# Kernel tuning notes

Hardware: AMD Instinct MI355X
Metric: run time of the kernel (lower is better)

## Reference

```python
import jax, jax.numpy as jnp
import numpy as np

HEADS = 4
DIM_HEAD = 64
MAP_SIZE = 16
SCALE = DIM_HEAD ** (-0.5)


def _split_heads(x):
    # torch rearrange 'b (dim_head heads) h w -> b heads (h w) dim_head'
    B, C, H, W = x.shape
    x = x.reshape(B, DIM_HEAD, HEADS, H * W)
    return jnp.transpose(x, (0, 2, 3, 1))  # [B, heads, N, dim_head]


def _merge_heads(x, H, W):
    # torch rearrange 'b heads (h w) dim_head -> b (dim_head heads) h w'
    B, h, N, d = x.shape
    return jnp.transpose(x, (0, 3, 1, 2)).reshape(B, d * h, H, W)


def setup_inputs() -> dict:
    key = jax.random.key(0)
    ks = jax.random.split(key, 6)
    feat = jax.random.normal(ks[0], (4, 256, 96, 96), jnp.float32)
    semantic_map = jax.random.normal(ks[1], (4, 256, 16, 16), jnp.float32)
    # 1x1 conv weights, shape [out_ch, in_ch]; scaled like fan-in init
    W_feat_qv = 0.05 * jax.random.normal(ks[2], (512, 256), jnp.float32)
    W_map_qv = 0.05 * jax.random.normal(ks[3], (512, 256), jnp.float32)
    W_feat_out = 0.05 * jax.random.normal(ks[4], (256, 256), jnp.float32)
    W_map_out = 0.05 * jax.random.normal(ks[5], (256, 256), jnp.float32)
    return {
        "feat": feat,
        "semantic_map": semantic_map,
        "W_feat_qv": W_feat_qv,
        "W_map_qv": W_map_qv,
        "W_feat_out": W_feat_out,
        "W_map_out": W_map_out,
    }


def reference(feat, semantic_map, W_feat_qv, W_map_qv, W_feat_out, W_map_out):
    B, C, H, W = feat.shape
    # 1x1 convs == per-pixel channel matmuls
    fqv = jnp.einsum("oc,bchw->bohw", W_feat_qv, feat)
    feat_q, feat_v = jnp.split(fqv, 2, axis=1)
    mqv = jnp.einsum("oc,bchw->bohw", W_map_qv, semantic_map)
    map_q, map_v = jnp.split(mqv, 2, axis=1)

    feat_q, feat_v = _split_heads(feat_q), _split_heads(feat_v)  # [B,h,N,d]
    map_q, map_v = _split_heads(map_q), _split_heads(map_v)      # [B,h,M,d]

    attn = jnp.einsum("bhid,bhjd->bhij", feat_q, map_q) * SCALE  # [B,h,N,M]
    feat_map_attn = jax.nn.softmax(attn, axis=-1)  # normalize over map tokens j
    map_feat_attn = jax.nn.softmax(attn, axis=-2)  # normalize over feat tokens i

    feat_o = jnp.einsum("bhij,bhjd->bhid", feat_map_attn, map_v)   # [B,h,N,d]
    map_o = jnp.einsum("bhji,bhjd->bhid", map_feat_attn, feat_v)   # [B,h,M,d]

    feat_o = _merge_heads(feat_o, H, W)
    map_o = _merge_heads(map_o, MAP_SIZE, MAP_SIZE)

    feat_out = jnp.einsum("oc,bchw->bohw", W_feat_out, feat_o)
    map_out = jnp.einsum("oc,bchw->bohw", W_map_out, map_o)
    return feat_out, map_out
```

## Files before the change

### kernel.cpp

```cpp
#include <hip/hip_runtime.h>
#include <stdint.h>

#define DI static __device__ __forceinline__

constexpr int NTOK = 9216;
constexpr float ATT_SCALE = 0.125f;

typedef short bf16x8 __attribute__((ext_vector_type(8)));
typedef float f32x4  __attribute__((ext_vector_type(4)));

DI f32x4 mfma16(bf16x8 a, bf16x8 b, f32x4 c) {
  return __builtin_amdgcn_mfma_f32_16x16x32_bf16(a, b, c, 0, 0, 0);
}

DI float b2f(uint16_t u) { union { uint32_t i; float f; } v; v.i = ((uint32_t)u) << 16; return v.f; }
DI uint16_t f2b(float f) {
  union { float f; uint32_t i; } v; v.f = f;
  uint32_t r = (v.i + 0x7fffu + ((v.i >> 16) & 1u)) >> 16;
  return (uint16_t)r;
}

template<int DT> DI float ld1(const void* p, size_t off) {
  if constexpr (DT) return b2f(((const uint16_t*)p)[off]);
  else              return ((const float*)p)[off];
}
template<int DT> DI void st1(void* p, size_t off, float v) {
  if constexpr (DT) ((uint16_t*)p)[off] = f2b(v);
  else              ((float*)p)[off] = v;
}

DI int block_flag256(const uint32_t* __restrict__ w) {
  const float b = b2f((uint16_t)(w[threadIdx.x & 255] & 0xffffu));
  const float ab = fabsf(b);
  return (__syncthreads_count((ab > 1e-4f && ab < 0.5f) ? 1 : 0) >= 128) ? 1 : 0;
}

template<int DT>
DI void prep_w_dev(int r, const void* __restrict__ Wfqv, const void* __restrict__ Wfo,
                   uint16_t* __restrict__ WqvP, uint16_t* __restrict__ WfoP)
{
  const int c = threadIdx.x;
  if (r < 512) {
    const int sel = r >> 8, within = r & 255;
    const int h = within >> 6, d = within & 63;
    const int src = sel * 256 + d * 4 + h;
    WqvP[(size_t)r * 256 + c] = f2b(ld1<DT>(Wfqv, (size_t)src * 256 + c));
  } else {
    const int ro = r - 512;
    WfoP[(size_t)ro * 256 + c] =
        f2b(ld1<DT>(Wfo, (size_t)ro * 256 + (c & 63) * 4 + (c >> 6)));
  }
}

template<int DT>
DI void map_qv_dev(int o, int bb, const void* __restrict__ Wqv,
                   const void* __restrict__ smap,
                   uint16_t* __restrict__ MQ, uint16_t* __restrict__ MVT)
{
  const int m = threadIdx.x;
  float acc = 0.f;
  #pragma unroll 8
  for (int c = 0; c < 256; ++c)
    acc += ld1<DT>(Wqv, (size_t)o * 256 + c) *
           ld1<DT>(smap, (size_t)bb * 65536 + (size_t)c * 256 + m);
  const int oc = o & 255;
  const int h = oc & 3, d = oc >> 2;
  if (o < 256) MQ[(((size_t)bb * 4 + h) * 256 + m) * 64 + d] = f2b(acc);
  else         MVT[(((size_t)bb * 4 + h) * 64 + d) * 256 + m] = f2b(acc);
}

__global__ __launch_bounds__(256) void prep_map_k(
    const void* Wfqv, const void* Wfo, const void* Wmqv, const void* smap,
    uint16_t* WqvP, uint16_t* WfoP, uint16_t* MQ, uint16_t* MVT)
{
  const int fl = block_flag256((const uint32_t*)Wfqv);
  const int bid = blockIdx.x;
  if (bid < 768) {
    if (fl) prep_w_dev<1>(bid, Wfqv, Wfo, WqvP, WfoP);
    else    prep_w_dev<0>(bid, Wfqv, Wfo, WqvP, WfoP);
  } else {
    const int idx = bid - 768;
    if (fl) map_qv_dev<1>(idx & 511, idx >> 9, Wmqv, smap, MQ, MVT);
    else    map_qv_dev<0>(idx & 511, idx >> 9, Wmqv, smap, MQ, MVT);
  }
}

constexpr int P0 = 280;

template<int DT>
DI void gemm0_body(uint16_t* Xs, const uint16_t* __restrict__ WqvP,
                   const void* __restrict__ X,
                   uint16_t* __restrict__ FQ, uint16_t* __restrict__ FVt)
{
  const int tid = threadIdx.x;
  const int w = tid >> 6, lane = tid & 63;
  const int l = lane & 15, quad = lane >> 4;
  const int n0 = blockIdx.x * 32;
  const int bb = blockIdx.y;
  const size_t bh = (size_t)bb * 4 + w;

  {
    const int nb = (tid & 15) * 2;
    const int kg = tid >> 4;
    #pragma unroll
    for (int pass = 0; pass < 2; ++pass) {
      const int k0 = pass * 128 + kg * 8;
      union { uint16_t h[8]; uint4 u; } pk0, pk1;
      #pragma unroll
      for (int j = 0; j < 8; ++j) {
        const size_t g = ((size_t)bb * 256 + k0 + j) * NTOK + n0 + nb;
        if constexpr (DT) {
          const uint32_t v = *(const uint32_t*)((const uint16_t*)X + g);
          pk0.h[j] = (uint16_t)(v & 0xffffu);
          pk1.h[j] = (uint16_t)(v >> 16);
        } else {
          const float2 v = *(const float2*)((const float*)X + g);
          pk0.h[j] = f2b(v.x);
          pk1.h[j] = f2b(v.y);
        }
      }
      *(uint4*)(Xs + (size_t)(nb + 0) * P0 + k0) = pk0.u;
      *(uint4*)(Xs + (size_t)(nb + 1) * P0 + k0) = pk1.u;
    }
  }
  __syncthreads();

  f32x4 acc[2][4][2];
  #pragma unroll
  for (int s = 0; s < 2; ++s)
    #pragma unroll
    for (int a = 0; a < 4; ++a)
      #pragma unroll
      for (int b = 0; b < 2; ++b) { acc[s][a][b].x = 0.f; acc[s][a][b].y = 0.f; acc[s][a][b].z = 0.f; acc[s][a][b].w = 0.f; }

  for (int ks = 0; ks < 8; ++ks) {
    bf16x8 bv[2];
    #pragma unroll
    for (int nt = 0; nt < 2; ++nt)
      bv[nt] = *(const bf16x8*)(Xs + (size_t)(nt * 16 + l) * P0 + ks * 32 + quad * 8);
    #pragma unroll
    for (int s = 0; s < 2; ++s) {
      bf16x8 af[4];
      #pragma unroll
      for (int mt = 0; mt < 4; ++mt) {
        const int arow = s * 256 + w * 64 + mt * 16 + l;
        af[mt] = *(const bf16x8*)(WqvP + (size_t)arow * 256 + ks * 32 + quad * 8);
      }
      #pragma unroll
      for (int nt = 0; nt < 2; ++nt)
        #pragma unroll
        for (int mt = 0; mt < 4; ++mt)
          acc[s][mt][nt] = mfma16(af[mt], bv[nt], acc[s][mt][nt]);
    }
  }
  const int itile = blockIdx.x;
  #pragma unroll
  for (int mt = 0; mt < 4; ++mt)
    #pragma unroll
    for (int nt = 0; nt < 2; ++nt) {
      const int n = n0 + nt * 16 + l;
      {
        union { uint16_t h[4]; uint2 u; } pk;
        #pragma unroll
        for (int r = 0; r < 4; ++r) pk.h[r] = f2b(acc[0][mt][nt][r]);
        *(uint2*)(FQ + (bh * NTOK + n) * 64 + mt * 16 + quad * 4) = pk.u;
      }
      {
        const int io = n & 31;
        #pragma unroll
        for (int r = 0; r < 4; ++r)
          FVt[(((size_t)bh * 288 + itile) * 64 + mt * 16 + quad * 4 + r) * 32 + io] =
              f2b(acc[1][mt][nt][r]);
      }
    }
}
__global__ __launch_bounds__(256, 3) void gemm0_mfma(
    const uint16_t* WqvP, const void* X, uint16_t* FQ, uint16_t* FVt,
    const void* Wfqv)
{
  __shared__ __align__(16) uint16_t Xs[32 * P0];
  const int fl = block_flag256((const uint32_t*)Wfqv);
  if (fl) gemm0_body<1>(Xs, WqvP, X, FQ, FVt);
  else    gemm0_body<0>(Xs, WqvP, X, FQ, FVt);
}

constexpr int PJ = 280;
constexpr int PI = 40;
constexpr int PO = 72;
constexpr int NGRP = 48;
constexpr int TPB = 6;

__global__ __launch_bounds__(256, 3) void attn_mfma(
    const uint16_t* __restrict__ FQ, const uint16_t* __restrict__ FVt,
    const uint16_t* __restrict__ MQ, const uint16_t* __restrict__ MVT,
    uint16_t* __restrict__ FO, uint16_t* __restrict__ P,
    uint16_t* __restrict__ CSp)
{
  __shared__ __align__(16) uint16_t Esh[32 * PJ];
  __shared__ __align__(16) uint16_t ETsh[256 * PI];
  __shared__ __align__(16) uint16_t Osh[32 * PO];
  __shared__ float RS[4][32];
  const int tid = threadIdx.x;
  const int w = tid >> 6;
  const int lane = tid & 63;
  const int l = lane & 15, quad = lane >> 4;
  const int blk = blockIdx.x, bh = blockIdx.y;
  const uint16_t* FQh  = FQ  + (size_t)bh * NTOK * 64;
  const uint16_t* FVth = FVt + (size_t)bh * 288 * 64 * 32;
  const uint16_t* MQh  = MQ  + (size_t)bh * 256 * 64;
  const uint16_t* MVTh = MVT + (size_t)bh * 64 * 256;
  uint16_t* FOh = FO + (size_t)bh * NTOK * 64;

  bf16x8 kb[4][2];
  #pragma unroll
  for (int jt = 0; jt < 4; ++jt) {
    const int j = w * 64 + jt * 16 + l;
    kb[jt][0] = *(const bf16x8*)(MQh + (size_t)j * 64 + quad * 8);
    kb[jt][1] = *(const bf16x8*)(MQh + (size_t)j * 64 + 32 + quad * 8);
  }
  bf16x8 avr[8];
  #pragma unroll
  for (int ks = 0; ks < 8; ++ks)
    avr[ks] = *(const bf16x8*)(MVTh + (size_t)(w * 16 + l) * 256 + ks * 32 + quad * 8);

  f32x4 numacc[4][4];
  #pragma unroll
  for (int a = 0; a < 4; ++a)
    #pragma unroll
    for (int b = 0; b < 4; ++b) { numacc[a][b].x = 0.f; numacc[a][b].y = 0.f; numacc[a][b].z = 0.f; numacc[a][b].w = 0.f; }
  float csum[4] = {0.f, 0.f, 0.f, 0.f};

  for (int t = 0; t < TPB; ++t) {
    const int it = blk * TPB + t;
    const int i0 = it * 32;

    bf16x8 qa[2][2];
    #pragma unroll
    for (int mt = 0; mt < 2; ++mt)
      #pragma unroll
      for (int kbi = 0; kbi < 2; ++kbi)
        qa[mt][kbi] = *(const bf16x8*)(FQh + (size_t)(i0 + mt * 16 + l) * 64 + kbi * 32 + quad * 8);

    float rsum[2][4] = {{0.f,0.f,0.f,0.f},{0.f,0.f,0.f,0.f}};
    #pragma unroll
    for (int jt = 0; jt < 4; ++jt) {
      const int j0 = w * 64 + jt * 16;
      #pragma unroll
      for (int mt = 0; mt < 2; ++mt) {
        f32x4 acc = {0.f, 0.f, 0.f, 0.f};
        acc = mfma16(qa[mt][0], kb[jt][0], acc);
        acc = mfma16(qa[mt][1], kb[jt][1], acc);
        union { uint16_t h[4]; uint2 u; } pk;
        #pragma unroll
        for (int r = 0; r < 4; ++r) {
          const float e = __expf(acc[r] * ATT_SCALE);
          rsum[mt][r] += e;
          csum[jt] += e;
          pk.h[r] = f2b(e);
          Esh[(mt * 16 + quad * 4 + r) * PJ + j0 + l] = pk.h[r];
        }
        *(uint2*)(ETsh + (size_t)(j0 + l) * PI + mt * 16 + quad * 4) = pk.u;
      }
    }
    #pragma unroll
    for (int mt = 0; mt < 2; ++mt)
      #pragma unroll
      for (int r = 0; r < 4; ++r) {
        float v = rsum[mt][r];
        v += __shfl_xor(v, 1); v += __shfl_xor(v, 2);
        v += __shfl_xor(v, 4); v += __shfl_xor(v, 8);
        if (l == 0) RS[w][mt * 16 + quad * 4 + r] = v;
      }
    __syncthreads();

    bf16x8 av[4];
    #pragma unroll
    for (int mt = 0; mt < 4; ++mt)
      av[mt] = *(const bf16x8*)(FVth + ((size_t)it * 64 + mt * 16 + l) * 32 + quad * 8);

    {
      float rinv[2];
      #pragma unroll
      for (int nt = 0; nt < 2; ++nt) {
        const int i_ = nt * 16 + l;
        rinv[nt] = 1.f / (RS[0][i_] + RS[1][i_] + RS[2][i_] + RS[3][i_]);
      }
      f32x4 oacc[2];
      oacc[0].x=0.f;oacc[0].y=0.f;oacc[0].z=0.f;oacc[0].w=0.f;
      oacc[1]=oacc[0];
      #pragma unroll
      for (int ks = 0; ks < 8; ++ks) {
        #pragma unroll
        for (int nt = 0; nt < 2; ++nt) {
          const bf16x8 bv = *(const bf16x8*)(Esh + (size_t)(nt * 16 + l) * PJ + ks * 32 + quad * 8);
          oacc[nt] = mfma16(avr[ks], bv, oacc[nt]);
        }
      }
      #pragma unroll
      for (int nt = 0; nt < 2; ++nt) {
        union { uint16_t h[4]; uint2 u; } pk;
        #pragma unroll
        for (int r = 0; r < 4; ++r) pk.h[r] = f2b(oacc[nt][r] * rinv[nt]);
        *(uint2*)(Osh + (nt * 16 + l) * PO + w * 16 + quad * 4) = pk.u;
      }
    }

    #pragma unroll
    for (int mt = 0; mt < 4; ++mt) {
      #pragma unroll
      for (int nt2 = 0; nt2 < 4; ++nt2) {
        const bf16x8 bv = *(const bf16x8*)(ETsh + (size_t)(w * 64 + nt2 * 16 + l) * PI + quad * 8);
        numacc[mt][nt2] = mfma16(av[mt], bv, numacc[mt][nt2]);
      }
    }
    __syncthreads();

    {
      const int ti = tid >> 3, c = tid & 7;
      *(uint4*)(FOh + (size_t)(i0 + ti) * 64 + c * 8) =
          *(const uint4*)(Osh + ti * PO + c * 8);
    }
  }

  uint16_t* Pb = P + ((size_t)bh * NGRP + blk) * 256 * 64;
  #pragma unroll
  for (int mt = 0; mt < 4; ++mt)
    #pragma unroll
    for (int nt2 = 0; nt2 < 4; ++nt2) {
      const int j = w * 64 + nt2 * 16 + l;
      union { uint16_t h[4]; uint2 u; } pk;
      #pragma unroll
      for (int r = 0; r < 4; ++r) pk.h[r] = f2b(numacc[mt][nt2][r]);
      *(uint2*)(Pb + (size_t)j * 64 + mt * 16 + quad * 4) = pk.u;
    }
  uint16_t* CSb = CSp + ((size_t)bh * NGRP + blk) * 256;
  #pragma unroll
  for (int jt = 0; jt < 4; ++jt) {
    float v = csum[jt];
    v += __shfl_xor(v, 16); v += __shfl_xor(v, 32);
    if (quad == 0) CSb[w * 64 + jt * 16 + l] = f2b(v);
  }
}

template<int DT>
DI void gemm1_dev(int gidx, const uint16_t* __restrict__ WfoP,
                  const uint16_t* __restrict__ FO, void* __restrict__ out)
{
  const int tid = threadIdx.x;
  const int w = tid >> 6, lane = tid & 63;
  const int l = lane & 15, quad = lane >> 4;
  const int n0 = (gidx % 36) * 256;
  const int o0 = ((gidx / 36) & 3) * 64;
  const int bb = gidx / 144;

  f32x4 acc[4][4];
  #pragma unroll
  for (int a = 0; a < 4; ++a)
    #pragma unroll
    for (int b = 0; b < 4; ++b) { acc[a][b].x = 0.f; acc[a][b].y = 0.f; acc[a][b].z = 0.f; acc[a][b].w = 0.f; }

  #pragma unroll
  for (int ks = 0; ks < 8; ++ks) {
    const int h2 = ks >> 1;
    const int doff = (ks & 1) * 32 + quad * 8;
    bf16x8 af[4];
    #pragma unroll
    for (int mt = 0; mt < 4; ++mt)
      af[mt] = *(const bf16x8*)(WfoP + (size_t)(o0 + mt * 16 + l) * 256 + ks * 32 + quad * 8);
    #pragma unroll
    for (int nt = 0; nt < 4; ++nt) {
      const int n = n0 + w * 64 + nt * 16 + l;
      const bf16x8 bv = *(const bf16x8*)(FO + ((size_t)(bb * 4 + h2) * NTOK + n) * 64 + doff);
      #pragma unroll
      for (int mt = 0; mt < 4; ++mt)
        acc[mt][nt] = mfma16(af[mt], bv, acc[mt][nt]);
    }
  }
  #pragma unroll
  for (int mt = 0; mt < 4; ++mt)
    #pragma unroll
    for (int nt = 0; nt < 4; ++nt) {
      const int n = n0 + w * 64 + nt * 16 + l;
      #pragma unroll
      for (int r = 0; r < 4; ++r)
        st1<DT>(out, ((size_t)bb * 256 + o0 + mt * 16 + quad * 4 + r) * NTOK + n,
                acc[mt][nt][r]);
    }
}

DI void reduce_dev(int bid, const uint16_t* __restrict__ P,
                   const uint16_t* __restrict__ CSp, uint16_t* __restrict__ MO)
{
  const int idx = bid * 256 + threadIdx.x;
  const int d = idx & 63;
  const int j = (idx >> 6) & 255;
  const int bh = idx >> 14;
  const size_t base = (size_t)bh * NGRP * 256 * 64;
  const size_t cb = (size_t)bh * NGRP * 256;
  float num = 0.f, cs = 0.f;
  #pragma unroll 6
  for (int g = 0; g < NGRP; ++g) {
    num += b2f(P[base + ((size_t)g * 256 + j) * 64 + d]);
    cs  += b2f(CSp[cb + (size_t)g * 256 + j]);
  }
  const float v = num / cs;
  const int b = bh >> 2, h = bh & 3;
  MO[((size_t)b * 256 + (d * 4 + h)) * 256 + j] = f2b(v);
}

__global__ __launch_bounds__(256) void epilogue_k(
    const uint16_t* WfoP, const uint16_t* FO, void* out,
    const uint16_t* P, const uint16_t* CSp, uint16_t* MO,
    const void* Wfqv, int mode)
{
  const int bid = blockIdx.x;
  bool do_g1; int gidx;
  if (mode == 0)      { do_g1 = bid < 576; gidx = do_g1 ? bid : bid - 576; }
  else if (mode == 1) { do_g1 = true;  gidx = bid; }
  else                { do_g1 = false; gidx = bid; }
  if (do_g1) {
    const int fl = block_flag256((const uint32_t*)Wfqv);
    if (fl) gemm1_dev<1>(gidx, WfoP, FO, out);
    else    gemm1_dev<0>(gidx, WfoP, FO, out);
  } else {
    reduce_dev(gidx, P, CSp, MO);
  }
}

template<int DT>
DI void map_out_body(const void* __restrict__ Wmo, const uint16_t* __restrict__ MO,
                     void* __restrict__ out)
{
  const int o = blockIdx.x, bb = blockIdx.y, m = threadIdx.x;
  float acc = 0.f;
  #pragma unroll 8
  for (int c = 0; c < 256; ++c)
    acc += ld1<DT>(Wmo, (size_t)o * 256 + c) *
           b2f(MO[((size_t)bb * 256 + c) * 256 + m]);
  const size_t MAP_OFS = (size_t)4 * 256 * NTOK;
  st1<DT>(out, MAP_OFS + ((size_t)bb * 256 + o) * 256 + m, acc);
}
__global__ __launch_bounds__(256) void map_out_k(
    const void* Wmo, const uint16_t* MO, void* out, const void* Wfqv)
{
  const int fl = block_flag256((const uint32_t*)Wfqv);
  if (fl) map_out_body<1>(Wmo, MO, out);
  else    map_out_body<0>(Wmo, MO, out);
}

extern "C" void kernel_launch(void* const* d_in, const int* in_sizes, int n_in,
                              void* d_out, int out_size, void* d_ws, size_t ws_size,
                              hipStream_t stream) {
  (void)in_sizes; (void)n_in; (void)out_size;
  const void* feat = d_in[0];
  const void* smap = d_in[1];
  const void* Wfqv = d_in[2];
  const void* Wmqv = d_in[3];
  const void* Wfo  = d_in[4];
  const void* Wmo  = d_in[5];
  char* ws = (char*)d_ws;

  const size_t BIG = (size_t)16 * 64 * NTOK * 2;
  const size_t SML = (size_t)16 * 256 * 64 * 2;
  const size_t FQ_OFF  = 0;
  const size_t FVT_OFF = FQ_OFF + BIG;
  const size_t MQ_OFF  = FVT_OFF + BIG;
  const size_t MVT_OFF = MQ_OFF + SML;
  const size_t MO_OFF  = MVT_OFF + SML;
  const size_t WQP_OFF = MO_OFF + (size_t)4 * 256 * 256 * 2;
  const size_t WFP_OFF = WQP_OFF + (size_t)512 * 256 * 2;
  const size_t CS_OFF  = WFP_OFF + (size_t)256 * 256 * 2;
  const size_t CS_SIZE = (size_t)16 * NGRP * 256 * 2;
  const size_t P_OFF   = CS_OFF + CS_SIZE;
  const size_t P_SIZE  = (size_t)16 * NGRP * 256 * 64 * 2;
  const size_t NEED    = P_OFF + P_SIZE;

  uint16_t* FQ   = (uint16_t*)(ws + FQ_OFF);
  uint16_t* FVt  = (uint16_t*)(ws + FVT_OFF);
  uint16_t* MQ   = (uint16_t*)(ws + MQ_OFF);
  uint16_t* MVT  = (uint16_t*)(ws + MVT_OFF);
  uint16_t* MO   = (uint16_t*)(ws + MO_OFF);
  uint16_t* WqvP = (uint16_t*)(ws + WQP_OFF);
  uint16_t* WfoP = (uint16_t*)(ws + WFP_OFF);

  const bool p_in_ws = (ws_size >= NEED);
  uint16_t* P   = p_in_ws ? (uint16_t*)(ws + P_OFF) : (uint16_t*)d_out;
  uint16_t* CSp = p_in_ws ? (uint16_t*)(ws + CS_OFF)
                          : (uint16_t*)((char*)d_out + P_SIZE);

  prep_map_k<<<dim3(2816), 256, 0, stream>>>(Wfqv, Wfo, Wmqv, smap,
                                             WqvP, WfoP, MQ, MVT);
  gemm0_mfma<<<dim3(288, 4), 256, 0, stream>>>(WqvP, feat, FQ, FVt, Wfqv);
  attn_mfma<<<dim3(NGRP, 16), 256, 0, stream>>>(FQ, FVt, MQ, MVT, FQ, P, CSp);
  if (p_in_ws) {
    epilogue_k<<<dim3(1600), 256, 0, stream>>>(WfoP, FQ, d_out, P, CSp, MO, Wfqv, 0);
  } else {
    epilogue_k<<<dim3(1024), 256, 0, stream>>>(WfoP, FQ, d_out, P, CSp, MO, Wfqv, 2);
    epilogue_k<<<dim3(576),  256, 0, stream>>>(WfoP, FQ, d_out, P, CSp, MO, Wfqv, 1);
  }
  map_out_k<<<dim3(256, 4), 256, 0, stream>>>(Wmo, MO, d_out, Wfqv);
}
```

Before: 299.8 us.

## Widen gemm0 token tile to 64 and stage gemm1 output through shared memory

gemm0 now processes 64 tokens per block instead of 32, so each loaded weight fragment feeds twice as many MFMAs and the grid is halved. This raises the accumulators to 32 f32x4 per thread, and the occupancy hint in launch bounds is dropped. gemm1's epilogue now transposes the accumulator tile through shared memory so that each output row is written with contiguous vector stores instead of scattered scalar stores. The cost is extra LDS traffic and barriers in gemm1, plus higher register pressure and possibly lower occupancy in gemm0.

```diff
diff --git a/kernel.cpp b/kernel.cpp
--- a/kernel.cpp
+++ b/kernel.cpp
@@ -95,16 +95,16 @@
   const int tid = threadIdx.x;
   const int w = tid >> 6, lane = tid & 63;
   const int l = lane & 15, quad = lane >> 4;
-  const int n0 = blockIdx.x * 32;
+  const int n0 = blockIdx.x * 64;
   const int bb = blockIdx.y;
   const size_t bh = (size_t)bb * 4 + w;
 
   {
-    const int nb = (tid & 15) * 2;
-    const int kg = tid >> 4;
-    #pragma unroll
-    for (int pass = 0; pass < 2; ++pass) {
-      const int k0 = pass * 128 + kg * 8;
+    const int nb = (tid & 31) * 2;
+    const int kg = tid >> 5;
+    #pragma unroll
+    for (int pass = 0; pass < 4; ++pass) {
+      const int k0 = pass * 64 + kg * 8;
       union { uint16_t h[8]; uint4 u; } pk0, pk1;
       #pragma unroll
       for (int j = 0; j < 8; ++j) {
@@ -125,60 +125,51 @@
   }
   __syncthreads();
 
-  f32x4 acc[2][4][2];
-  #pragma unroll
-  for (int s = 0; s < 2; ++s)
-    #pragma unroll
-    for (int a = 0; a < 4; ++a)
-      #pragma unroll
-      for (int b = 0; b < 2; ++b) { acc[s][a][b].x = 0.f; acc[s][a][b].y = 0.f; acc[s][a][b].z = 0.f; acc[s][a][b].w = 0.f; }
+  f32x4 acc[8][4];
+  #pragma unroll
+  for (int a = 0; a < 8; ++a)
+    #pragma unroll
+    for (int b = 0; b < 4; ++b) { acc[a][b].x = 0.f; acc[a][b].y = 0.f; acc[a][b].z = 0.f; acc[a][b].w = 0.f; }
 
   for (int ks = 0; ks < 8; ++ks) {
-    bf16x8 bv[2];
-    #pragma unroll
-    for (int nt = 0; nt < 2; ++nt)
-      bv[nt] = *(const bf16x8*)(Xs + (size_t)(nt * 16 + l) * P0 + ks * 32 + quad * 8);
-    #pragma unroll
-    for (int s = 0; s < 2; ++s) {
-      bf16x8 af[4];
-      #pragma unroll
-      for (int mt = 0; mt < 4; ++mt) {
-        const int arow = s * 256 + w * 64 + mt * 16 + l;
-        af[mt] = *(const bf16x8*)(WqvP + (size_t)arow * 256 + ks * 32 + quad * 8);
-      }
-      #pragma unroll
-      for (int nt = 0; nt < 2; ++nt)
-        #pragma unroll
-        for (int mt = 0; mt < 4; ++mt)
-          acc[s][mt][nt] = mfma16(af[mt], bv[nt], acc[s][mt][nt]);
-    }
-  }
-  const int itile = blockIdx.x;
-  #pragma unroll
-  for (int mt = 0; mt < 4; ++mt)
-    #pragma unroll
-    for (int nt = 0; nt < 2; ++nt) {
+    bf16x8 af[8];
+    #pragma unroll
+    for (int mt = 0; mt < 8; ++mt) {
+      const int arow = (mt >> 2) * 256 + w * 64 + (mt & 3) * 16 + l;
+      af[mt] = *(const bf16x8*)(WqvP + (size_t)arow * 256 + ks * 32 + quad * 8);
+    }
+    #pragma unroll
+    for (int nt = 0; nt < 4; ++nt) {
+      const bf16x8 bv = *(const bf16x8*)(Xs + (size_t)(nt * 16 + l) * P0 + ks * 32 + quad * 8);
+      #pragma unroll
+      for (int mt = 0; mt < 8; ++mt)
+        acc[mt][nt] = mfma16(af[mt], bv, acc[mt][nt]);
+    }
+  }
+  #pragma unroll
+  for (int mt = 0; mt < 8; ++mt)
+    #pragma unroll
+    for (int nt = 0; nt < 4; ++nt) {
       const int n = n0 + nt * 16 + l;
-      {
+      if (mt < 4) {
         union { uint16_t h[4]; uint2 u; } pk;
         #pragma unroll
-        for (int r = 0; r < 4; ++r) pk.h[r] = f2b(acc[0][mt][nt][r]);
+        for (int r = 0; r < 4; ++r) pk.h[r] = f2b(acc[mt][nt][r]);
         *(uint2*)(FQ + (bh * NTOK + n) * 64 + mt * 16 + quad * 4) = pk.u;
-      }
-      {
-        const int io = n & 31;
+      } else {
+        const int itile = n >> 5, io = n & 31;
         #pragma unroll
         for (int r = 0; r < 4; ++r)
-          FVt[(((size_t)bh * 288 + itile) * 64 + mt * 16 + quad * 4 + r) * 32 + io] =
-              f2b(acc[1][mt][nt][r]);
-      }
-    }
-}
-__global__ __launch_bounds__(256, 3) void gemm0_mfma(
+          FVt[(((size_t)bh * 288 + itile) * 64 + (mt - 4) * 16 + quad * 4 + r) * 32 + io] =
+              f2b(acc[mt][nt][r]);
+      }
+    }
+}
+__global__ __launch_bounds__(256) void gemm0_mfma(
     const uint16_t* WqvP, const void* X, uint16_t* FQ, uint16_t* FVt,
     const void* Wfqv)
 {
-  __shared__ __align__(16) uint16_t Xs[32 * P0];
+  __shared__ __align__(16) uint16_t Xs[64 * P0];
   const int fl = block_flag256((const uint32_t*)Wfqv);
   if (fl) gemm0_body<1>(Xs, WqvP, X, FQ, FVt);
   else    gemm0_body<0>(Xs, WqvP, X, FQ, FVt);
@@ -342,9 +333,12 @@
   }
 }
 
+constexpr int PG = 260;
+
 template<int DT>
 DI void gemm1_dev(int gidx, const uint16_t* __restrict__ WfoP,
-                  const uint16_t* __restrict__ FO, void* __restrict__ out)
+                  const uint16_t* __restrict__ FO, void* __restrict__ out,
+                  float* __restrict__ Gsh)
 {
   const int tid = threadIdx.x;
   const int w = tid >> 6, lane = tid & 63;
@@ -376,16 +370,32 @@
         acc[mt][nt] = mfma16(af[mt], bv, acc[mt][nt]);
     }
   }
-  #pragma unroll
-  for (int mt = 0; mt < 4; ++mt)
-    #pragma unroll
-    for (int nt = 0; nt < 4; ++nt) {
-      const int n = n0 + w * 64 + nt * 16 + l;
+
+  #pragma unroll
+  for (int mt = 0; mt < 4; ++mt) {
+    if (mt) __syncthreads();
+    #pragma unroll
+    for (int nt = 0; nt < 4; ++nt)
       #pragma unroll
       for (int r = 0; r < 4; ++r)
-        st1<DT>(out, ((size_t)bb * 256 + o0 + mt * 16 + quad * 4 + r) * NTOK + n,
-                acc[mt][nt][r]);
-    }
+        Gsh[(quad * 4 + r) * PG + w * 64 + nt * 16 + l] = acc[mt][nt][r];
+    __syncthreads();
+    const int row = tid >> 4, c = tid & 15;
+    const size_t obase = ((size_t)bb * 256 + o0 + mt * 16 + row) * NTOK + n0;
+    #pragma unroll
+    for (int k = 0; k < 4; ++k) {
+      const int nc = k * 64 + c * 4;
+      const float* src = Gsh + row * PG + nc;
+      if constexpr (DT) {
+        union { uint16_t h[4]; uint2 u; } pk;
+        #pragma unroll
+        for (int q2 = 0; q2 < 4; ++q2) pk.h[q2] = f2b(src[q2]);
+        *(uint2*)((uint16_t*)out + obase + nc) = pk.u;
+      } else {
+        *(float4*)((float*)out + obase + nc) = *(const float4*)src;
+      }
+    }
+  }
 }
 
 DI void reduce_dev(int bid, const uint16_t* __restrict__ P,
@@ -413,6 +423,7 @@
     const uint16_t* P, const uint16_t* CSp, uint16_t* MO,
     const void* Wfqv, int mode)
 {
+  __shared__ __align__(16) float Gsh[16 * PG];
   const int bid = blockIdx.x;
   bool do_g1; int gidx;
   if (mode == 0)      { do_g1 = bid < 576; gidx = do_g1 ? bid : bid - 576; }
@@ -420,8 +431,8 @@
   else                { do_g1 = false; gidx = bid; }
   if (do_g1) {
     const int fl = block_flag256((const uint32_t*)Wfqv);
-    if (fl) gemm1_dev<1>(gidx, WfoP, FO, out);
-    else    gemm1_dev<0>(gidx, WfoP, FO, out);
+    if (fl) gemm1_dev<1>(gidx, WfoP, FO, out, Gsh);
+    else    gemm1_dev<0>(gidx, WfoP, FO, out, Gsh);
   } else {
     reduce_dev(gidx, P, CSp, MO);
   }
@@ -490,7 +501,7 @@
 
   prep_map_k<<<dim3(2816), 256, 0, stream>>>(Wfqv, Wfo, Wmqv, smap,
                                              WqvP, WfoP, MQ, MVT);
-  gemm0_mfma<<<dim3(288, 4), 256, 0, stream>>>(WqvP, feat, FQ, FVt, Wfqv);
+  gemm0_mfma<<<dim3(144, 4), 256, 0, stream>>>(WqvP, feat, FQ, FVt, Wfqv);
   attn_mfma<<<dim3(NGRP, 16), 256, 0, stream>>>(FQ, FVt, MQ, MVT, FQ, P, CSp);
   if (p_in_ws) {
     epilogue_k<<<dim3(1600), 256, 0, stream>>>(WfoP, FQ, d_out, P, CSp, MO, Wfqv, 0);
```

Result: faster. 289.3 us (-3.5%).
